# Kernel optimization log

Measured on AMD Instinct MI355X. Metric: run time of the kernel, lower is better.

## Reference

```python
import jax, jax.numpy as jnp
import numpy as np

N_USERS = 200000
N_ITEMS = 100000
N_EDGES = 1000000
D = 64
NUM_LAYERS = 3
BATCH = 8192


def setup_inputs() -> dict:
    key = jax.random.key(0)
    ks = jax.random.split(key, 8)
    return {
        "user_feat": jax.random.normal(ks[0], (N_USERS, D), dtype=jnp.float32) * 0.1,
        "item_feat": jax.random.normal(ks[1], (N_ITEMS, D), dtype=jnp.float32) * 0.1,
        "edge_u": jax.random.randint(ks[2], (N_EDGES,), 0, N_USERS, dtype=jnp.int32),
        "edge_i": jax.random.randint(ks[3], (N_EDGES,), 0, N_ITEMS, dtype=jnp.int32),
        "norm": jax.random.uniform(ks[4], (N_EDGES,), dtype=jnp.float32),
        "users": jax.random.randint(ks[5], (BATCH,), 0, N_USERS, dtype=jnp.int32),
        "pos_items": jax.random.randint(ks[6], (BATCH,), 0, N_ITEMS, dtype=jnp.int32),
        "neg_items": jax.random.randint(ks[7], (BATCH,), 0, N_ITEMS, dtype=jnp.int32),
    }


def reference(user_feat, item_feat, edge_u, edge_i, norm, users, pos_items, neg_items):
    # LightGCN propagation: each layer does edge-weighted gather-scatter
    # (u_mul_e 'h','norm' -> sum) in both directions of the bipartite graph.
    u_h, i_h = user_feat, item_feat
    u_acc, i_acc = u_h, i_h
    w = norm[:, None]  # [E, 1]
    for _ in range(NUM_LAYERS):
        # user -> item messages
        new_i = jax.ops.segment_sum(u_h[edge_u] * w, edge_i, num_segments=N_ITEMS)
        # item -> user messages
        new_u = jax.ops.segment_sum(i_h[edge_i] * w, edge_u, num_segments=N_USERS)
        u_h, i_h = new_u, new_i
        u_acc = u_acc + u_h
        i_acc = i_acc + i_h
    scale = 1.0 / (NUM_LAYERS + 1)
    u_acc = u_acc * scale
    i_acc = i_acc * scale
    return (u_acc[users], i_acc[pos_items], i_acc[neg_items])
```

## Files before the change

### kernel.cpp

```cpp
#include <hip/hip_runtime.h>


#define N_USERS 200000
#define N_ITEMS 100000
#define N_EDGES 1000000
#define DIM 64
#define BATCH 8192
#define NTOT (N_USERS + N_ITEMS)
#define NOUT (3 * BATCH)
#define NPART 293
#define PLOCAL 1024

#define HA 489
#define CB (NTOT * DIM / 8 / 256)
#define OB (NOUT * 16 / 256)
#define AB (NTOT / 16)
#define FB ((NOUT + 255) / 256)

__device__ __forceinline__ unsigned f2bf(float f) {
    unsigned u = __float_as_uint(f);
    return (u + 0x7fffu + ((u >> 16) & 1u)) >> 16;
}
__device__ __forceinline__ uint2 pack4(float4 v) {
    uint2 o;
    o.x = f2bf(v.x) | (f2bf(v.y) << 16);
    o.y = f2bf(v.z) | (f2bf(v.w) << 16);
    return o;
}
__device__ __forceinline__ void fma4(float4& a, uint2 v, float w) {
    a.x += __uint_as_float(v.x << 16) * w;
    a.y += __uint_as_float(v.x & 0xffff0000u) * w;
    a.z += __uint_as_float(v.y << 16) * w;
    a.w += __uint_as_float(v.y & 0xffff0000u) * w;
}
__device__ __forceinline__ int out_bucket(int orow, const int* users,
                                          const int* pos, const int* neg) {
    int seg = orow >> 13;
    int b = orow & (BATCH - 1);
    if (seg == 0) return users[b];
    if (seg == 1) return N_USERS + pos[b];
    return N_USERS + neg[b];
}

__global__ void fused_pre_kernel(const int* __restrict__ eu,
                                 const int* __restrict__ ei,
                                 int* __restrict__ partTotals,
                                 const float4* __restrict__ uf4,
                                 const float4* __restrict__ if4,
                                 unsigned short* __restrict__ F0,
                                 const float* __restrict__ u_feat,
                                 const float* __restrict__ i_feat,
                                 const int* __restrict__ users,
                                 const int* __restrict__ pos,
                                 const int* __restrict__ neg,
                                 float* __restrict__ out)
{
    __shared__ int lh[NPART];
    int bid = blockIdx.x;
    if (bid < HA) {
        for (int k = threadIdx.x; k < NPART; k += 256) lh[k] = 0;
        __syncthreads();
        int e0 = (bid * 256 + threadIdx.x) * 8;
        if (e0 < N_EDGES) {
            int4 u0 = *reinterpret_cast<const int4*>(eu + e0);
            int4 u1 = *reinterpret_cast<const int4*>(eu + e0 + 4);
            int4 i0 = *reinterpret_cast<const int4*>(ei + e0);
            int4 i1 = *reinterpret_cast<const int4*>(ei + e0 + 4);
            atomicAdd(&lh[u0.x >> 10], 1);
            atomicAdd(&lh[u0.y >> 10], 1);
            atomicAdd(&lh[u0.z >> 10], 1);
            atomicAdd(&lh[u0.w >> 10], 1);
            atomicAdd(&lh[u1.x >> 10], 1);
            atomicAdd(&lh[u1.y >> 10], 1);
            atomicAdd(&lh[u1.z >> 10], 1);
            atomicAdd(&lh[u1.w >> 10], 1);
            atomicAdd(&lh[(N_USERS + i0.x) >> 10], 1);
            atomicAdd(&lh[(N_USERS + i0.y) >> 10], 1);
            atomicAdd(&lh[(N_USERS + i0.z) >> 10], 1);
            atomicAdd(&lh[(N_USERS + i0.w) >> 10], 1);
            atomicAdd(&lh[(N_USERS + i1.x) >> 10], 1);
            atomicAdd(&lh[(N_USERS + i1.y) >> 10], 1);
            atomicAdd(&lh[(N_USERS + i1.z) >> 10], 1);
            atomicAdd(&lh[(N_USERS + i1.w) >> 10], 1);
        }
        __syncthreads();
        for (int k = threadIdx.x; k < NPART; k += 256) {
            int v = lh[k];
            if (v) atomicAdd(&partTotals[k], v);
        }
    } else if (bid < HA + CB) {
        int j = (bid - HA) * 256 + threadIdx.x;
        int f4 = j * 2;
        const int NU4 = N_USERS * DIM / 4;
        float4 a, b;
        if (f4 < NU4) { a = uf4[f4]; b = uf4[f4 + 1]; }
        else          { a = if4[f4 - NU4]; b = if4[f4 - NU4 + 1]; }
        uint2 pa = pack4(a), pb = pack4(b);
        *reinterpret_cast<uint4*>(F0 + (size_t)j * 8) =
            make_uint4(pa.x, pa.y, pb.x, pb.y);
    } else {
        int idx = (bid - HA - CB) * 256 + threadIdx.x;
        int row = idx >> 4;
        if (row >= NOUT) return;
        int d4 = (idx & 15) << 2;
        int seg = row >> 13;
        int b = row & (BATCH - 1);
        const float* src;
        if (seg == 0)      src = u_feat + (size_t)users[b] * DIM;
        else if (seg == 1) src = i_feat + (size_t)pos[b]   * DIM;
        else               src = i_feat + (size_t)neg[b]   * DIM;
        float4 v = *reinterpret_cast<const float4*>(src + d4);
        v.x *= 0.25f; v.y *= 0.25f; v.z *= 0.25f; v.w *= 0.25f;
        *reinterpret_cast<float4*>(out + (size_t)row * DIM + d4) = v;
    }
}

__global__ void part_scan_kernel(const int* __restrict__ partTotals,
                                 int* __restrict__ partStart,
                                 int* __restrict__ gcur)
{
    __shared__ int s[512];
    int t = threadIdx.x;
    s[t] = (t < NPART) ? partTotals[t] : 0;
    __syncthreads();
    for (int off = 1; off < 512; off <<= 1) {
        int x = (t >= off) ? s[t - off] : 0;
        __syncthreads();
        s[t] += x;
        __syncthreads();
    }
    if (t < NPART) {
        int st = (t == 0) ? 0 : s[t - 1];
        partStart[t] = st;
        gcur[t] = st;
    }
    if (t == NPART) partStart[NPART] = s[NPART - 1];
}

__global__ void partition_kernel(const int* __restrict__ eu,
                                 const int* __restrict__ ei,
                                 const float* __restrict__ w,
                                 int* __restrict__ gcur,
                                 uint2* __restrict__ partBuf)
{
    __shared__ int lh[NPART];
    __shared__ int lcur[NPART];
    int bid = blockIdx.x, t = threadIdx.x;
    for (int k = t; k < NPART; k += 256) lh[k] = 0;
    __syncthreads();
    int e0 = (bid * 256 + t) * 8;
    bool act = e0 < N_EDGES;
    int4 u0, u1, i0, i1;
    if (act) {
        u0 = *reinterpret_cast<const int4*>(eu + e0);
        u1 = *reinterpret_cast<const int4*>(eu + e0 + 4);
        i0 = *reinterpret_cast<const int4*>(ei + e0);
        i1 = *reinterpret_cast<const int4*>(ei + e0 + 4);
        atomicAdd(&lh[u0.x >> 10], 1);
        atomicAdd(&lh[u0.y >> 10], 1);
        atomicAdd(&lh[u0.z >> 10], 1);
        atomicAdd(&lh[u0.w >> 10], 1);
        atomicAdd(&lh[u1.x >> 10], 1);
        atomicAdd(&lh[u1.y >> 10], 1);
        atomicAdd(&lh[u1.z >> 10], 1);
        atomicAdd(&lh[u1.w >> 10], 1);
        atomicAdd(&lh[(N_USERS + i0.x) >> 10], 1);
        atomicAdd(&lh[(N_USERS + i0.y) >> 10], 1);
        atomicAdd(&lh[(N_USERS + i0.z) >> 10], 1);
        atomicAdd(&lh[(N_USERS + i0.w) >> 10], 1);
        atomicAdd(&lh[(N_USERS + i1.x) >> 10], 1);
        atomicAdd(&lh[(N_USERS + i1.y) >> 10], 1);
        atomicAdd(&lh[(N_USERS + i1.z) >> 10], 1);
        atomicAdd(&lh[(N_USERS + i1.w) >> 10], 1);
    }
    __syncthreads();
    for (int k = t; k < NPART; k += 256) {
        int v = lh[k];
        lcur[k] = v ? atomicAdd(&gcur[k], v) : 0;
    }
    __syncthreads();
    if (act) {
        float4 wa = *reinterpret_cast<const float4*>(w + e0);
        float4 wb = *reinterpret_cast<const float4*>(w + e0 + 4);
        int us[8] = {u0.x, u0.y, u0.z, u0.w, u1.x, u1.y, u1.z, u1.w};
        int is[8] = {i0.x, i0.y, i0.z, i0.w, i1.x, i1.y, i1.z, i1.w};
        float ws[8] = {wa.x, wa.y, wa.z, wa.w, wb.x, wb.y, wb.z, wb.w};
        #pragma unroll
        for (int j = 0; j < 8; ++j) {
            int bu = us[j];
            int bi = N_USERS + is[j];
            unsigned wbits = __float_as_uint(ws[j]);
            int su = atomicAdd(&lcur[bu >> 10], 1);
            partBuf[su] = make_uint2((unsigned)(bu & 1023) | ((unsigned)bi << 10), wbits);
            int si = atomicAdd(&lcur[bi >> 10], 1);
            partBuf[si] = make_uint2((unsigned)(bi & 1023) | ((unsigned)bu << 10), wbits);
        }
    }
}

__global__ void build_csr_kernel(const int* __restrict__ partStart,
                                 const uint2* __restrict__ partBuf,
                                 int* __restrict__ rp,
                                 int2* __restrict__ entries)
{
    __shared__ int h[PLOCAL];
    __shared__ int cur[PLOCAL];
    __shared__ int s[256];
    int p = blockIdx.x, t = threadIdx.x;
    int base = partStart[p], end = partStart[p + 1];
    h[t * 4 + 0] = 0; h[t * 4 + 1] = 0; h[t * 4 + 2] = 0; h[t * 4 + 3] = 0;
    __syncthreads();
    for (int r = base + t; r < end; r += 256)
        atomicAdd(&h[partBuf[r].x & 1023], 1);
    __syncthreads();
    int h0 = h[t * 4], h1 = h[t * 4 + 1], h2 = h[t * 4 + 2], h3 = h[t * 4 + 3];
    s[t] = h0 + h1 + h2 + h3;
    __syncthreads();
    for (int off = 1; off < 256; off <<= 1) {
        int x = (t >= off) ? s[t - off] : 0;
        __syncthreads();
        s[t] += x;
        __syncthreads();
    }
    int b0 = base + ((t == 0) ? 0 : s[t - 1]);
    cur[t * 4 + 0] = b0;
    cur[t * 4 + 1] = b0 + h0;
    cur[t * 4 + 2] = b0 + h0 + h1;
    cur[t * 4 + 3] = b0 + h0 + h1 + h2;
    int gb = p * PLOCAL + t * 4;
    #pragma unroll
    for (int k = 0; k < 4; ++k)
        if (gb + k <= NTOT) rp[gb + k] = cur[t * 4 + k];
    __syncthreads();
    for (int r = base + t; r < end; r += 256) {
        uint2 rec = partBuf[r];
        int b = rec.x & 1023;
        int col = rec.x >> 10;
        int slot = atomicAdd(&cur[b], 1);
        entries[slot] = make_int2(col, (int)rec.y);
    }
}

#define GATH(idx, acc)                                                        \
    {                                                                         \
        int c = __shfl(e.x, qb + (idx));                                      \
        float ww = __int_as_float(__shfl(e.y, qb + (idx)));                   \
        uint2 v = *reinterpret_cast<const uint2*>(                            \
            src + (size_t)c * DIM + l16 * 4);                                 \
        fma4(acc, v, ww);                                                     \
    }

__device__ __forceinline__ void agg_row(int row, int l16, int quad,
                                        const int* __restrict__ rp,
                                        const int2* __restrict__ entries,
                                        const unsigned short* __restrict__ src,
                                        float4& s)
{
    int beg = rp[row];
    int end = rp[row + 1];
    int cnt = end - beg;
    int qb = quad << 4;
    float4 a0 = {0,0,0,0}, a1 = {0,0,0,0}, a2 = {0,0,0,0}, a3 = {0,0,0,0};
    for (int base = 0; base < cnt; base += 16) {
        int rem = min(16, cnt - base);
        int2 e = make_int2(0, 0);
        if (l16 < rem) e = entries[beg + base + l16];
        int j = 0;
        for (; j + 7 < rem; j += 8) {
            GATH(j + 0, a0) GATH(j + 1, a1) GATH(j + 2, a2) GATH(j + 3, a3)
            GATH(j + 4, a0) GATH(j + 5, a1) GATH(j + 6, a2) GATH(j + 7, a3)
        }
        if (j + 3 < rem) {
            GATH(j + 0, a0) GATH(j + 1, a1) GATH(j + 2, a2) GATH(j + 3, a3)
            j += 4;
        }
        if (j + 1 < rem) {
            GATH(j + 0, a0) GATH(j + 1, a1)
            j += 2;
        }
        if (j < rem) GATH(j, a2)
    }
    s.x = (a0.x + a1.x) + (a2.x + a3.x);
    s.y = (a0.y + a1.y) + (a2.y + a3.y);
    s.z = (a0.z + a1.z) + (a2.z + a3.z);
    s.w = (a0.w + a1.w) + (a2.w + a3.w);
}

__global__ void agg1_flag_kernel(const int* __restrict__ rp,
                                 const int2* __restrict__ entries,
                                 const unsigned short* __restrict__ F0,
                                 unsigned short* __restrict__ H1,
                                 const int* __restrict__ users,
                                 const int* __restrict__ pos,
                                 const int* __restrict__ neg,
                                 int* __restrict__ flags)
{
    int bid = blockIdx.x;
    if (bid < AB) {
        int gid = bid * 256 + threadIdx.x;
        int lane = gid & 63;
        int quad = lane >> 4;
        int l16 = lane & 15;
        int row = (gid >> 6) * 4 + quad;
        if (row >= NTOT) return;
        float4 s;
        agg_row(row, l16, quad, rp, entries, F0, s);
        *reinterpret_cast<uint2*>(H1 + (size_t)row * DIM + l16 * 4) = pack4(s);
    } else {
        int t = (bid - AB) * 256 + threadIdx.x;
        if (t >= NOUT) return;
        int bucket = out_bucket(t, users, pos, neg);
        flags[bucket] = 1;
        int beg = rp[bucket], end = rp[bucket + 1];
        for (int k = beg; k < end; ++k)
            flags[entries[k].x] = 1;
    }
}

__global__ void compact_kernel(const int* __restrict__ flags,
                               int* __restrict__ list,
                               int* __restrict__ count)
{
    int t = blockIdx.x * blockDim.x + threadIdx.x;
    int idx = t * 4;
    if (idx >= NTOT) return;
    int4 f = *reinterpret_cast<const int4*>(flags + idx);
    int loc[4]; int k = 0;
    if (f.x) loc[k++] = idx;
    if (f.y) loc[k++] = idx + 1;
    if (f.z) loc[k++] = idx + 2;
    if (f.w) loc[k++] = idx + 3;
    if (k) {
        int base = atomicAdd(count, k);
        for (int m = 0; m < k; ++m) list[base + m] = loc[m];
    }
}

__global__ void agg2_add1_kernel(const int* __restrict__ rp,
                                 const int2* __restrict__ entries,
                                 const unsigned short* __restrict__ H1,
                                 unsigned short* __restrict__ H2,
                                 const int* __restrict__ list,
                                 const int* __restrict__ count,
                                 const int* __restrict__ users,
                                 const int* __restrict__ pos,
                                 const int* __restrict__ neg,
                                 float* __restrict__ out)
{
    int bid = blockIdx.x;
    if (bid < AB) {
        int gid = bid * 256 + threadIdx.x;
        int lane = gid & 63;
        int quad = lane >> 4;
        int l16 = lane & 15;
        int idx4 = (gid >> 6) * 4 + quad;
        int n = *count;
        if (idx4 >= n) return;
        int row = list[idx4];
        float4 s;
        agg_row(row, l16, quad, rp, entries, H1, s);
        *reinterpret_cast<uint2*>(H2 + (size_t)row * DIM + l16 * 4) = pack4(s);
    } else {
        int idx = (bid - AB) * 256 + threadIdx.x;
        int row = idx >> 4;
        if (row >= NOUT) return;
        int d4 = (idx & 15) << 2;
        int bucket = out_bucket(row, users, pos, neg);
        uint2 v = *reinterpret_cast<const uint2*>(H1 + (size_t)bucket * DIM + d4);
        float* op = out + (size_t)row * DIM + d4;
        float4 o = *reinterpret_cast<const float4*>(op);
        o.x += 0.25f * __uint_as_float(v.x << 16);
        o.y += 0.25f * __uint_as_float(v.x & 0xffff0000u);
        o.z += 0.25f * __uint_as_float(v.y << 16);
        o.w += 0.25f * __uint_as_float(v.y & 0xffff0000u);
        *reinterpret_cast<float4*>(op) = o;
    }
}

__global__ void aggout_add2_kernel(const int* __restrict__ rp,
                                   const int2* __restrict__ entries,
                                   const unsigned short* __restrict__ H2,
                                   const int* __restrict__ users,
                                   const int* __restrict__ pos,
                                   const int* __restrict__ neg,
                                   float* __restrict__ out)
{
    int gid = blockIdx.x * 256 + threadIdx.x;
    int lane = gid & 63;
    int quad = lane >> 4;
    int l16 = lane & 15;
    int orow = (gid >> 6) * 4 + quad;
    if (orow >= NOUT) return;
    int bucket = out_bucket(orow, users, pos, neg);
    float4 s;
    agg_row(bucket, l16, quad, rp, entries, H2, s);
    uint2 v = *reinterpret_cast<const uint2*>(H2 + (size_t)bucket * DIM + l16 * 4);
    s.x += __uint_as_float(v.x << 16);
    s.y += __uint_as_float(v.x & 0xffff0000u);
    s.z += __uint_as_float(v.y << 16);
    s.w += __uint_as_float(v.y & 0xffff0000u);
    float* op = out + (size_t)orow * DIM + l16 * 4;
    float4 o = *reinterpret_cast<const float4*>(op);
    o.x += 0.25f * s.x; o.y += 0.25f * s.y;
    o.z += 0.25f * s.z; o.w += 0.25f * s.w;
    *reinterpret_cast<float4*>(op) = o;
}

extern "C" void kernel_launch(void* const* d_in, const int* in_sizes, int n_in,
                              void* d_out, int out_size, void* d_ws, size_t ws_size,
                              hipStream_t stream)
{
    const float* user_feat = (const float*)d_in[0];
    const float* item_feat = (const float*)d_in[1];
    const int*   eu        = (const int*)d_in[2];
    const int*   ei        = (const int*)d_in[3];
    const float* norm      = (const float*)d_in[4];
    const int*   users     = (const int*)d_in[5];
    const int*   pos       = (const int*)d_in[6];
    const int*   neg       = (const int*)d_in[7];
    float* out = (float*)d_out;

    auto align256 = [](size_t x) { return (x + 255) & ~(size_t)255; };
    const size_t hBytes = (size_t)NTOT * DIM * sizeof(unsigned short);

    char* p = (char*)d_ws;
    unsigned short* F0 = (unsigned short*)p; p += align256(hBytes);
    unsigned short* H1 = (unsigned short*)p; p += align256(hBytes);
    unsigned short* H2 = (unsigned short*)p; p += align256(hBytes);
    int* partTotals = (int*)p; p += align256((size_t)(512 + NTOT + 16) * 4);
    int* flags = partTotals + 512;
    int* count = flags + NTOT;
    int*  partStart = (int*)p;  p += align256(512 * 4);
    int*  gcur      = (int*)p;  p += align256(512 * 4);
    int*  rp        = (int*)p;  p += align256((size_t)(NTOT + 1) * 4);
    uint2* partBuf  = (uint2*)p; p += align256((size_t)2 * N_EDGES * 8);
    int*  list      = (int*)p;  p += align256((size_t)NTOT * 4);
    int2* entries   = (int2*)p; p += align256((size_t)2 * N_EDGES * 8);

    hipMemsetAsync(partTotals, 0, (size_t)(512 + NTOT + 16) * 4, stream);

    fused_pre_kernel<<<HA + CB + OB, 256, 0, stream>>>(
        eu, ei, partTotals,
        (const float4*)user_feat, (const float4*)item_feat, F0,
        user_feat, item_feat, users, pos, neg, out);

    part_scan_kernel<<<1, 512, 0, stream>>>(partTotals, partStart, gcur);

    partition_kernel<<<HA, 256, 0, stream>>>(eu, ei, norm, gcur, partBuf);

    build_csr_kernel<<<NPART, 256, 0, stream>>>(partStart, partBuf, rp, entries);

    agg1_flag_kernel<<<AB + FB, 256, 0, stream>>>(
        rp, entries, F0, H1, users, pos, neg, flags);

    compact_kernel<<<(NTOT / 4 + 255) / 256, 256, 0, stream>>>(flags, list, count);

    agg2_add1_kernel<<<AB + OB, 256, 0, stream>>>(
        rp, entries, H1, H2, list, count, users, pos, neg, out);

    aggout_add2_kernel<<<NOUT / 16, 256, 0, stream>>>(
        rp, entries, H2, users, pos, neg, out);
}
```

Measured before the change: 312.0 us.

## Move frontier flagging into partition, fuse compaction into CSR build, widen gathers

Output buckets are now marked in a bitmap inside the preprocessing kernel. Their neighbours are flagged by an extra half of the partition grid that scans the raw edge list, so the flagging no longer runs in the first aggregation kernel. Compaction of flagged rows is fused into the CSR build launch, which removes one kernel launch. The aggregation kernels now assign 8 lanes per row with 16-byte bf16 loads instead of 16 lanes with 8-byte loads, giving fewer shuffles and wider memory transactions per row. In exchange, the memset grows and the flagging pass reads every edge once more with random bitmap lookups.

```diff
diff --git a/kernel.cpp b/kernel.cpp
--- a/kernel.cpp
+++ b/kernel.cpp
@@ -14,8 +14,9 @@
 #define HA 489
 #define CB (NTOT * DIM / 8 / 256)
 #define OB (NOUT * 16 / 256)
-#define AB (NTOT / 16)
-#define FB ((NOUT + 255) / 256)
+#define BB ((NOUT + 255) / 256)
+#define AB8 (NTOT / 32)
+#define CPB ((NTOT / 4 + 255) / 256)
 
 __device__ __forceinline__ unsigned f2bf(float f) {
     unsigned u = __float_as_uint(f);
@@ -27,11 +28,15 @@
     o.y = f2bf(v.z) | (f2bf(v.w) << 16);
     return o;
 }
-__device__ __forceinline__ void fma4(float4& a, uint2 v, float w) {
+__device__ __forceinline__ void fma8(float4& a, float4& b, uint4 v, float w) {
     a.x += __uint_as_float(v.x << 16) * w;
     a.y += __uint_as_float(v.x & 0xffff0000u) * w;
     a.z += __uint_as_float(v.y << 16) * w;
     a.w += __uint_as_float(v.y & 0xffff0000u) * w;
+    b.x += __uint_as_float(v.z << 16) * w;
+    b.y += __uint_as_float(v.z & 0xffff0000u) * w;
+    b.z += __uint_as_float(v.w << 16) * w;
+    b.w += __uint_as_float(v.w & 0xffff0000u) * w;
 }
 __device__ __forceinline__ int out_bucket(int orow, const int* users,
                                           const int* pos, const int* neg) {
@@ -53,7 +58,9 @@
                                  const int* __restrict__ users,
                                  const int* __restrict__ pos,
                                  const int* __restrict__ neg,
-                                 float* __restrict__ out)
+                                 float* __restrict__ out,
+                                 int* __restrict__ bitmap,
+                                 int* __restrict__ flags)
 {
     __shared__ int lh[NPART];
     int bid = blockIdx.x;
@@ -98,7 +105,7 @@
         uint2 pa = pack4(a), pb = pack4(b);
         *reinterpret_cast<uint4*>(F0 + (size_t)j * 8) =
             make_uint4(pa.x, pa.y, pb.x, pb.y);
-    } else {
+    } else if (bid < HA + CB + OB) {
         int idx = (bid - HA - CB) * 256 + threadIdx.x;
         int row = idx >> 4;
         if (row >= NOUT) return;
@@ -112,6 +119,12 @@
         float4 v = *reinterpret_cast<const float4*>(src + d4);
         v.x *= 0.25f; v.y *= 0.25f; v.z *= 0.25f; v.w *= 0.25f;
         *reinterpret_cast<float4*>(out + (size_t)row * DIM + d4) = v;
+    } else {
+        int t = (bid - HA - CB - OB) * 256 + threadIdx.x;
+        if (t >= NOUT) return;
+        int bucket = out_bucket(t, users, pos, neg);
+        bitmap[bucket] = 1;
+        flags[bucket] = 1;
     }
 }
 
@@ -141,59 +154,77 @@
                                  const int* __restrict__ ei,
                                  const float* __restrict__ w,
                                  int* __restrict__ gcur,
-                                 uint2* __restrict__ partBuf)
+                                 uint2* __restrict__ partBuf,
+                                 const int* __restrict__ bitmap,
+                                 int* __restrict__ flags)
 {
     __shared__ int lh[NPART];
     __shared__ int lcur[NPART];
     int bid = blockIdx.x, t = threadIdx.x;
-    for (int k = t; k < NPART; k += 256) lh[k] = 0;
-    __syncthreads();
-    int e0 = (bid * 256 + t) * 8;
-    bool act = e0 < N_EDGES;
-    int4 u0, u1, i0, i1;
-    if (act) {
-        u0 = *reinterpret_cast<const int4*>(eu + e0);
-        u1 = *reinterpret_cast<const int4*>(eu + e0 + 4);
-        i0 = *reinterpret_cast<const int4*>(ei + e0);
-        i1 = *reinterpret_cast<const int4*>(ei + e0 + 4);
-        atomicAdd(&lh[u0.x >> 10], 1);
-        atomicAdd(&lh[u0.y >> 10], 1);
-        atomicAdd(&lh[u0.z >> 10], 1);
-        atomicAdd(&lh[u0.w >> 10], 1);
-        atomicAdd(&lh[u1.x >> 10], 1);
-        atomicAdd(&lh[u1.y >> 10], 1);
-        atomicAdd(&lh[u1.z >> 10], 1);
-        atomicAdd(&lh[u1.w >> 10], 1);
-        atomicAdd(&lh[(N_USERS + i0.x) >> 10], 1);
-        atomicAdd(&lh[(N_USERS + i0.y) >> 10], 1);
-        atomicAdd(&lh[(N_USERS + i0.z) >> 10], 1);
-        atomicAdd(&lh[(N_USERS + i0.w) >> 10], 1);
-        atomicAdd(&lh[(N_USERS + i1.x) >> 10], 1);
-        atomicAdd(&lh[(N_USERS + i1.y) >> 10], 1);
-        atomicAdd(&lh[(N_USERS + i1.z) >> 10], 1);
-        atomicAdd(&lh[(N_USERS + i1.w) >> 10], 1);
-    }
-    __syncthreads();
-    for (int k = t; k < NPART; k += 256) {
-        int v = lh[k];
-        lcur[k] = v ? atomicAdd(&gcur[k], v) : 0;
-    }
-    __syncthreads();
-    if (act) {
-        float4 wa = *reinterpret_cast<const float4*>(w + e0);
-        float4 wb = *reinterpret_cast<const float4*>(w + e0 + 4);
+    if (bid < HA) {
+        for (int k = t; k < NPART; k += 256) lh[k] = 0;
+        __syncthreads();
+        int e0 = (bid * 256 + t) * 8;
+        bool act = e0 < N_EDGES;
+        int4 u0, u1, i0, i1;
+        if (act) {
+            u0 = *reinterpret_cast<const int4*>(eu + e0);
+            u1 = *reinterpret_cast<const int4*>(eu + e0 + 4);
+            i0 = *reinterpret_cast<const int4*>(ei + e0);
+            i1 = *reinterpret_cast<const int4*>(ei + e0 + 4);
+            atomicAdd(&lh[u0.x >> 10], 1);
+            atomicAdd(&lh[u0.y >> 10], 1);
+            atomicAdd(&lh[u0.z >> 10], 1);
+            atomicAdd(&lh[u0.w >> 10], 1);
+            atomicAdd(&lh[u1.x >> 10], 1);
+            atomicAdd(&lh[u1.y >> 10], 1);
+            atomicAdd(&lh[u1.z >> 10], 1);
+            atomicAdd(&lh[u1.w >> 10], 1);
+            atomicAdd(&lh[(N_USERS + i0.x) >> 10], 1);
+            atomicAdd(&lh[(N_USERS + i0.y) >> 10], 1);
+            atomicAdd(&lh[(N_USERS + i0.z) >> 10], 1);
+            atomicAdd(&lh[(N_USERS + i0.w) >> 10], 1);
+            atomicAdd(&lh[(N_USERS + i1.x) >> 10], 1);
+            atomicAdd(&lh[(N_USERS + i1.y) >> 10], 1);
+            atomicAdd(&lh[(N_USERS + i1.z) >> 10], 1);
+            atomicAdd(&lh[(N_USERS + i1.w) >> 10], 1);
+        }
+        __syncthreads();
+        for (int k = t; k < NPART; k += 256) {
+            int v = lh[k];
+            lcur[k] = v ? atomicAdd(&gcur[k], v) : 0;
+        }
+        __syncthreads();
+        if (act) {
+            float4 wa = *reinterpret_cast<const float4*>(w + e0);
+            float4 wb = *reinterpret_cast<const float4*>(w + e0 + 4);
+            int us[8] = {u0.x, u0.y, u0.z, u0.w, u1.x, u1.y, u1.z, u1.w};
+            int is[8] = {i0.x, i0.y, i0.z, i0.w, i1.x, i1.y, i1.z, i1.w};
+            float ws[8] = {wa.x, wa.y, wa.z, wa.w, wb.x, wb.y, wb.z, wb.w};
+            #pragma unroll
+            for (int j = 0; j < 8; ++j) {
+                int bu = us[j];
+                int bi = N_USERS + is[j];
+                unsigned wbits = __float_as_uint(ws[j]);
+                int su = atomicAdd(&lcur[bu >> 10], 1);
+                partBuf[su] = make_uint2((unsigned)(bu & 1023) | ((unsigned)bi << 10), wbits);
+                int si = atomicAdd(&lcur[bi >> 10], 1);
+                partBuf[si] = make_uint2((unsigned)(bi & 1023) | ((unsigned)bu << 10), wbits);
+            }
+        }
+    } else {
+        int e0 = ((bid - HA) * 256 + t) * 8;
+        if (e0 >= N_EDGES) return;
+        int4 u0 = *reinterpret_cast<const int4*>(eu + e0);
+        int4 u1 = *reinterpret_cast<const int4*>(eu + e0 + 4);
+        int4 i0 = *reinterpret_cast<const int4*>(ei + e0);
+        int4 i1 = *reinterpret_cast<const int4*>(ei + e0 + 4);
         int us[8] = {u0.x, u0.y, u0.z, u0.w, u1.x, u1.y, u1.z, u1.w};
         int is[8] = {i0.x, i0.y, i0.z, i0.w, i1.x, i1.y, i1.z, i1.w};
-        float ws[8] = {wa.x, wa.y, wa.z, wa.w, wb.x, wb.y, wb.z, wb.w};
         #pragma unroll
         for (int j = 0; j < 8; ++j) {
-            int bu = us[j];
-            int bi = N_USERS + is[j];
-            unsigned wbits = __float_as_uint(ws[j]);
-            int su = atomicAdd(&lcur[bu >> 10], 1);
-            partBuf[su] = make_uint2((unsigned)(bu & 1023) | ((unsigned)bi << 10), wbits);
-            int si = atomicAdd(&lcur[bi >> 10], 1);
-            partBuf[si] = make_uint2((unsigned)(bi & 1023) | ((unsigned)bu << 10), wbits);
+            if (bitmap[us[j]]) flags[N_USERS + is[j]] = 1;
+            if (bitmap[N_USERS + is[j]]) flags[us[j]] = 1;
         }
     }
 }
@@ -201,139 +232,134 @@
 __global__ void build_csr_kernel(const int* __restrict__ partStart,
                                  const uint2* __restrict__ partBuf,
                                  int* __restrict__ rp,
-                                 int2* __restrict__ entries)
+                                 int2* __restrict__ entries,
+                                 const int* __restrict__ flags,
+                                 int* __restrict__ list,
+                                 int* __restrict__ count)
 {
     __shared__ int h[PLOCAL];
     __shared__ int cur[PLOCAL];
     __shared__ int s[256];
-    int p = blockIdx.x, t = threadIdx.x;
-    int base = partStart[p], end = partStart[p + 1];
-    h[t * 4 + 0] = 0; h[t * 4 + 1] = 0; h[t * 4 + 2] = 0; h[t * 4 + 3] = 0;
-    __syncthreads();
-    for (int r = base + t; r < end; r += 256)
-        atomicAdd(&h[partBuf[r].x & 1023], 1);
-    __syncthreads();
-    int h0 = h[t * 4], h1 = h[t * 4 + 1], h2 = h[t * 4 + 2], h3 = h[t * 4 + 3];
-    s[t] = h0 + h1 + h2 + h3;
-    __syncthreads();
-    for (int off = 1; off < 256; off <<= 1) {
-        int x = (t >= off) ? s[t - off] : 0;
-        __syncthreads();
-        s[t] += x;
-        __syncthreads();
-    }
-    int b0 = base + ((t == 0) ? 0 : s[t - 1]);
-    cur[t * 4 + 0] = b0;
-    cur[t * 4 + 1] = b0 + h0;
-    cur[t * 4 + 2] = b0 + h0 + h1;
-    cur[t * 4 + 3] = b0 + h0 + h1 + h2;
-    int gb = p * PLOCAL + t * 4;
-    #pragma unroll
-    for (int k = 0; k < 4; ++k)
-        if (gb + k <= NTOT) rp[gb + k] = cur[t * 4 + k];
-    __syncthreads();
-    for (int r = base + t; r < end; r += 256) {
-        uint2 rec = partBuf[r];
-        int b = rec.x & 1023;
-        int col = rec.x >> 10;
-        int slot = atomicAdd(&cur[b], 1);
-        entries[slot] = make_int2(col, (int)rec.y);
-    }
-}
-
-#define GATH(idx, acc)                                                        \
+    int t = threadIdx.x;
+    if (blockIdx.x < NPART) {
+        int p = blockIdx.x;
+        int base = partStart[p], end = partStart[p + 1];
+        h[t * 4 + 0] = 0; h[t * 4 + 1] = 0; h[t * 4 + 2] = 0; h[t * 4 + 3] = 0;
+        __syncthreads();
+        for (int r = base + t; r < end; r += 256)
+            atomicAdd(&h[partBuf[r].x & 1023], 1);
+        __syncthreads();
+        int h0 = h[t * 4], h1 = h[t * 4 + 1], h2 = h[t * 4 + 2], h3 = h[t * 4 + 3];
+        s[t] = h0 + h1 + h2 + h3;
+        __syncthreads();
+        for (int off = 1; off < 256; off <<= 1) {
+            int x = (t >= off) ? s[t - off] : 0;
+            __syncthreads();
+            s[t] += x;
+            __syncthreads();
+        }
+        int b0 = base + ((t == 0) ? 0 : s[t - 1]);
+        cur[t * 4 + 0] = b0;
+        cur[t * 4 + 1] = b0 + h0;
+        cur[t * 4 + 2] = b0 + h0 + h1;
+        cur[t * 4 + 3] = b0 + h0 + h1 + h2;
+        int gb = p * PLOCAL + t * 4;
+        #pragma unroll
+        for (int k = 0; k < 4; ++k)
+            if (gb + k <= NTOT) rp[gb + k] = cur[t * 4 + k];
+        __syncthreads();
+        for (int r = base + t; r < end; r += 256) {
+            uint2 rec = partBuf[r];
+            int b = rec.x & 1023;
+            int col = rec.x >> 10;
+            int slot = atomicAdd(&cur[b], 1);
+            entries[slot] = make_int2(col, (int)rec.y);
+        }
+    } else {
+        int idx = ((blockIdx.x - NPART) * 256 + t) * 4;
+        if (idx >= NTOT) return;
+        int4 f = *reinterpret_cast<const int4*>(flags + idx);
+        int loc[4]; int k = 0;
+        if (f.x) loc[k++] = idx;
+        if (f.y) loc[k++] = idx + 1;
+        if (f.z) loc[k++] = idx + 2;
+        if (f.w) loc[k++] = idx + 3;
+        if (k) {
+            int base = atomicAdd(count, k);
+            for (int m = 0; m < k; ++m) list[base + m] = loc[m];
+        }
+    }
+}
+
+#define GATH8(idx, A, B)                                                      \
     {                                                                         \
         int c = __shfl(e.x, qb + (idx));                                      \
         float ww = __int_as_float(__shfl(e.y, qb + (idx)));                   \
-        uint2 v = *reinterpret_cast<const uint2*>(                            \
-            src + (size_t)c * DIM + l16 * 4);                                 \
-        fma4(acc, v, ww);                                                     \
-    }
-
-__device__ __forceinline__ void agg_row(int row, int l16, int quad,
-                                        const int* __restrict__ rp,
-                                        const int2* __restrict__ entries,
-                                        const unsigned short* __restrict__ src,
-                                        float4& s)
+        uint4 v = *reinterpret_cast<const uint4*>(                            \
+            src + (size_t)c * DIM + l8 * 8);                                  \
+        fma8(A, B, v, ww);                                                    \
+    }
+
+__device__ __forceinline__ void agg_row8(int row, int l8, int g8,
+                                         const int* __restrict__ rp,
+                                         const int2* __restrict__ entries,
+                                         const unsigned short* __restrict__ src,
+                                         float4& sa, float4& sb)
 {
     int beg = rp[row];
     int end = rp[row + 1];
     int cnt = end - beg;
-    int qb = quad << 4;
+    int qb = g8 << 3;
     float4 a0 = {0,0,0,0}, a1 = {0,0,0,0}, a2 = {0,0,0,0}, a3 = {0,0,0,0};
-    for (int base = 0; base < cnt; base += 16) {
-        int rem = min(16, cnt - base);
+    float4 b0 = {0,0,0,0}, b1 = {0,0,0,0}, b2 = {0,0,0,0}, b3 = {0,0,0,0};
+    for (int base = 0; base < cnt; base += 8) {
+        int rem = min(8, cnt - base);
         int2 e = make_int2(0, 0);
-        if (l16 < rem) e = entries[beg + base + l16];
+        if (l8 < rem) e = entries[beg + base + l8];
         int j = 0;
         for (; j + 7 < rem; j += 8) {
-            GATH(j + 0, a0) GATH(j + 1, a1) GATH(j + 2, a2) GATH(j + 3, a3)
-            GATH(j + 4, a0) GATH(j + 5, a1) GATH(j + 6, a2) GATH(j + 7, a3)
+            GATH8(j + 0, a0, b0) GATH8(j + 1, a1, b1)
+            GATH8(j + 2, a2, b2) GATH8(j + 3, a3, b3)
+            GATH8(j + 4, a0, b0) GATH8(j + 5, a1, b1)
+            GATH8(j + 6, a2, b2) GATH8(j + 7, a3, b3)
         }
         if (j + 3 < rem) {
-            GATH(j + 0, a0) GATH(j + 1, a1) GATH(j + 2, a2) GATH(j + 3, a3)
+            GATH8(j + 0, a0, b0) GATH8(j + 1, a1, b1)
+            GATH8(j + 2, a2, b2) GATH8(j + 3, a3, b3)
             j += 4;
         }
         if (j + 1 < rem) {
-            GATH(j + 0, a0) GATH(j + 1, a1)
+            GATH8(j + 0, a0, b0) GATH8(j + 1, a1, b1)
             j += 2;
         }
-        if (j < rem) GATH(j, a2)
-    }
-    s.x = (a0.x + a1.x) + (a2.x + a3.x);
-    s.y = (a0.y + a1.y) + (a2.y + a3.y);
-    s.z = (a0.z + a1.z) + (a2.z + a3.z);
-    s.w = (a0.w + a1.w) + (a2.w + a3.w);
-}
-
-__global__ void agg1_flag_kernel(const int* __restrict__ rp,
-                                 const int2* __restrict__ entries,
-                                 const unsigned short* __restrict__ F0,
-                                 unsigned short* __restrict__ H1,
-                                 const int* __restrict__ users,
-                                 const int* __restrict__ pos,
-                                 const int* __restrict__ neg,
-                                 int* __restrict__ flags)
-{
-    int bid = blockIdx.x;
-    if (bid < AB) {
-        int gid = bid * 256 + threadIdx.x;
-        int lane = gid & 63;
-        int quad = lane >> 4;
-        int l16 = lane & 15;
-        int row = (gid >> 6) * 4 + quad;
-        if (row >= NTOT) return;
-        float4 s;
-        agg_row(row, l16, quad, rp, entries, F0, s);
-        *reinterpret_cast<uint2*>(H1 + (size_t)row * DIM + l16 * 4) = pack4(s);
-    } else {
-        int t = (bid - AB) * 256 + threadIdx.x;
-        if (t >= NOUT) return;
-        int bucket = out_bucket(t, users, pos, neg);
-        flags[bucket] = 1;
-        int beg = rp[bucket], end = rp[bucket + 1];
-        for (int k = beg; k < end; ++k)
-            flags[entries[k].x] = 1;
-    }
-}
-
-__global__ void compact_kernel(const int* __restrict__ flags,
-                               int* __restrict__ list,
-                               int* __restrict__ count)
-{
-    int t = blockIdx.x * blockDim.x + threadIdx.x;
-    int idx = t * 4;
-    if (idx >= NTOT) return;
-    int4 f = *reinterpret_cast<const int4*>(flags + idx);
-    int loc[4]; int k = 0;
-    if (f.x) loc[k++] = idx;
-    if (f.y) loc[k++] = idx + 1;
-    if (f.z) loc[k++] = idx + 2;
-    if (f.w) loc[k++] = idx + 3;
-    if (k) {
-        int base = atomicAdd(count, k);
-        for (int m = 0; m < k; ++m) list[base + m] = loc[m];
-    }
+        if (j < rem) GATH8(j, a2, b2)
+    }
+    sa.x = (a0.x + a1.x) + (a2.x + a3.x);
+    sa.y = (a0.y + a1.y) + (a2.y + a3.y);
+    sa.z = (a0.z + a1.z) + (a2.z + a3.z);
+    sa.w = (a0.w + a1.w) + (a2.w + a3.w);
+    sb.x = (b0.x + b1.x) + (b2.x + b3.x);
+    sb.y = (b0.y + b1.y) + (b2.y + b3.y);
+    sb.z = (b0.z + b1.z) + (b2.z + b3.z);
+    sb.w = (b0.w + b1.w) + (b2.w + b3.w);
+}
+
+__global__ void agg1_kernel(const int* __restrict__ rp,
+                            const int2* __restrict__ entries,
+                            const unsigned short* __restrict__ F0,
+                            unsigned short* __restrict__ H1)
+{
+    int gid = blockIdx.x * 256 + threadIdx.x;
+    int lane = gid & 63;
+    int g8 = lane >> 3;
+    int l8 = lane & 7;
+    int row = (gid >> 6) * 8 + g8;
+    if (row >= NTOT) return;
+    float4 sa, sb;
+    agg_row8(row, l8, g8, rp, entries, F0, sa, sb);
+    uint2 pa = pack4(sa), pb = pack4(sb);
+    *reinterpret_cast<uint4*>(H1 + (size_t)row * DIM + l8 * 8) =
+        make_uint4(pa.x, pa.y, pb.x, pb.y);
 }
 
 __global__ void agg2_add1_kernel(const int* __restrict__ rp,
@@ -348,20 +374,22 @@
                                  float* __restrict__ out)
 {
     int bid = blockIdx.x;
-    if (bid < AB) {
+    if (bid < AB8) {
         int gid = bid * 256 + threadIdx.x;
         int lane = gid & 63;
-        int quad = lane >> 4;
-        int l16 = lane & 15;
-        int idx4 = (gid >> 6) * 4 + quad;
+        int g8 = lane >> 3;
+        int l8 = lane & 7;
+        int idx8 = (gid >> 6) * 8 + g8;
         int n = *count;
-        if (idx4 >= n) return;
-        int row = list[idx4];
-        float4 s;
-        agg_row(row, l16, quad, rp, entries, H1, s);
-        *reinterpret_cast<uint2*>(H2 + (size_t)row * DIM + l16 * 4) = pack4(s);
+        if (idx8 >= n) return;
+        int row = list[idx8];
+        float4 sa, sb;
+        agg_row8(row, l8, g8, rp, entries, H1, sa, sb);
+        uint2 pa = pack4(sa), pb = pack4(sb);
+        *reinterpret_cast<uint4*>(H2 + (size_t)row * DIM + l8 * 8) =
+            make_uint4(pa.x, pa.y, pb.x, pb.y);
     } else {
-        int idx = (bid - AB) * 256 + threadIdx.x;
+        int idx = (bid - AB8) * 256 + threadIdx.x;
         int row = idx >> 4;
         if (row >= NOUT) return;
         int d4 = (idx & 15) << 2;
@@ -387,23 +415,31 @@
 {
     int gid = blockIdx.x * 256 + threadIdx.x;
     int lane = gid & 63;
-    int quad = lane >> 4;
-    int l16 = lane & 15;
-    int orow = (gid >> 6) * 4 + quad;
+    int g8 = lane >> 3;
+    int l8 = lane & 7;
+    int orow = (gid >> 6) * 8 + g8;
     if (orow >= NOUT) return;
     int bucket = out_bucket(orow, users, pos, neg);
-    float4 s;
-    agg_row(bucket, l16, quad, rp, entries, H2, s);
-    uint2 v = *reinterpret_cast<const uint2*>(H2 + (size_t)bucket * DIM + l16 * 4);
-    s.x += __uint_as_float(v.x << 16);
-    s.y += __uint_as_float(v.x & 0xffff0000u);
-    s.z += __uint_as_float(v.y << 16);
-    s.w += __uint_as_float(v.y & 0xffff0000u);
-    float* op = out + (size_t)orow * DIM + l16 * 4;
-    float4 o = *reinterpret_cast<const float4*>(op);
-    o.x += 0.25f * s.x; o.y += 0.25f * s.y;
-    o.z += 0.25f * s.z; o.w += 0.25f * s.w;
-    *reinterpret_cast<float4*>(op) = o;
+    float4 sa, sb;
+    agg_row8(bucket, l8, g8, rp, entries, H2, sa, sb);
+    uint4 v = *reinterpret_cast<const uint4*>(H2 + (size_t)bucket * DIM + l8 * 8);
+    sa.x += __uint_as_float(v.x << 16);
+    sa.y += __uint_as_float(v.x & 0xffff0000u);
+    sa.z += __uint_as_float(v.y << 16);
+    sa.w += __uint_as_float(v.y & 0xffff0000u);
+    sb.x += __uint_as_float(v.z << 16);
+    sb.y += __uint_as_float(v.z & 0xffff0000u);
+    sb.z += __uint_as_float(v.w << 16);
+    sb.w += __uint_as_float(v.w & 0xffff0000u);
+    float* op = out + (size_t)orow * DIM + l8 * 8;
+    float4 o0 = *reinterpret_cast<const float4*>(op);
+    float4 o1 = *reinterpret_cast<const float4*>(op + 4);
+    o0.x += 0.25f * sa.x; o0.y += 0.25f * sa.y;
+    o0.z += 0.25f * sa.z; o0.w += 0.25f * sa.w;
+    o1.x += 0.25f * sb.x; o1.y += 0.25f * sb.y;
+    o1.z += 0.25f * sb.z; o1.w += 0.25f * sb.w;
+    *reinterpret_cast<float4*>(op) = o0;
+    *reinterpret_cast<float4*>(op + 4) = o1;
 }
 
 extern "C" void kernel_launch(void* const* d_in, const int* in_sizes, int n_in,
@@ -427,9 +463,10 @@
     unsigned short* F0 = (unsigned short*)p; p += align256(hBytes);
     unsigned short* H1 = (unsigned short*)p; p += align256(hBytes);
     unsigned short* H2 = (unsigned short*)p; p += align256(hBytes);
-    int* partTotals = (int*)p; p += align256((size_t)(512 + NTOT + 16) * 4);
-    int* flags = partTotals + 512;
-    int* count = flags + NTOT;
+    int* partTotals = (int*)p; p += align256((size_t)(512 + 2 * NTOT + 16) * 4);
+    int* bitmap = partTotals + 512;
+    int* flags  = bitmap + NTOT;
+    int* count  = flags + NTOT;
     int*  partStart = (int*)p;  p += align256(512 * 4);
     int*  gcur      = (int*)p;  p += align256(512 * 4);
     int*  rp        = (int*)p;  p += align256((size_t)(NTOT + 1) * 4);
@@ -437,27 +474,26 @@
     int*  list      = (int*)p;  p += align256((size_t)NTOT * 4);
     int2* entries   = (int2*)p; p += align256((size_t)2 * N_EDGES * 8);
 
-    hipMemsetAsync(partTotals, 0, (size_t)(512 + NTOT + 16) * 4, stream);
-
-    fused_pre_kernel<<<HA + CB + OB, 256, 0, stream>>>(
+    hipMemsetAsync(partTotals, 0, (size_t)(512 + 2 * NTOT + 16) * 4, stream);
+
+    fused_pre_kernel<<<HA + CB + OB + BB, 256, 0, stream>>>(
         eu, ei, partTotals,
         (const float4*)user_feat, (const float4*)item_feat, F0,
-        user_feat, item_feat, users, pos, neg, out);
+        user_feat, item_feat, users, pos, neg, out, bitmap, flags);
 
     part_scan_kernel<<<1, 512, 0, stream>>>(partTotals, partStart, gcur);
 
-    partition_kernel<<<HA, 256, 0, stream>>>(eu, ei, norm, gcur, partBuf);
-
-    build_csr_kernel<<<NPART, 256, 0, stream>>>(partStart, partBuf, rp, entries);
-
-    agg1_flag_kernel<<<AB + FB, 256, 0, stream>>>(
-        rp, entries, F0, H1, users, pos, neg, flags);
-
-    compact_kernel<<<(NTOT / 4 + 255) / 256, 256, 0, stream>>>(flags, list, count);
-
-    agg2_add1_kernel<<<AB + OB, 256, 0, stream>>>(
+    partition_kernel<<<HA + HA, 256, 0, stream>>>(
+        eu, ei, norm, gcur, partBuf, bitmap, flags);
+
+    build_csr_kernel<<<NPART + CPB, 256, 0, stream>>>(
+        partStart, partBuf, rp, entries, flags, list, count);
+
+    agg1_kernel<<<AB8, 256, 0, stream>>>(rp, entries, F0, H1);
+
+    agg2_add1_kernel<<<AB8 + OB, 256, 0, stream>>>(
         rp, entries, H1, H2, list, count, users, pos, neg, out);
 
-    aggout_add2_kernel<<<NOUT / 16, 256, 0, stream>>>(
+    aggout_add2_kernel<<<NOUT / 32, 256, 0, stream>>>(
         rp, entries, H2, users, pos, neg, out);
 }
```

Measured after the change: 321.3 us. +3.0%, slower.
